# Kernel tuning notes

Hardware: AMD Instinct MI355X
Metric: run time of the kernel (lower is better)

## Reference

```python
import jax, jax.numpy as jnp
import numpy as np
from jax.ops import segment_sum

N_NODES = 50000
N_EDGES = 800000
D = 128
N_LAYERS = 3
N_GRAPHS = 256


def setup_inputs() -> dict:
    key = jax.random.key(0)
    k1, k2, k3, k4, k5, k6 = jax.random.split(key, 6)
    feats = jax.random.normal(k1, (N_NODES, D), dtype=jnp.float32)
    src = jax.random.randint(k2, (N_EDGES,), 0, N_NODES)
    dst = jax.random.randint(k3, (N_EDGES,), 0, N_NODES)
    graph_ids = jnp.sort(jax.random.randint(k4, (N_NODES,), 0, N_GRAPHS))
    W = jax.random.normal(k5, (N_LAYERS, D, D), dtype=jnp.float32) / np.float32(np.sqrt(D))
    b = jax.random.normal(k6, (N_LAYERS, D), dtype=jnp.float32) * 0.01
    return {"feats": feats, "W": W, "b": b, "src": src, "dst": dst, "graph_ids": graph_ids}


def reference(feats, W, b, src, dst, graph_ids):
    # DGL GraphConv with norm='both': h' = act(D_in^{-1/2} A D_out^{-1/2} h W + b)
    ones_e = jnp.ones((src.shape[0],), dtype=feats.dtype)
    deg_out = jnp.clip(segment_sum(ones_e, src, num_segments=N_NODES), 1.0)  # [N]
    deg_in = jnp.clip(segment_sum(ones_e, dst, num_segments=N_NODES), 1.0)   # [N]
    norm_out = jax.lax.rsqrt(deg_out)[:, None]  # [N,1]
    norm_in = jax.lax.rsqrt(deg_in)[:, None]    # [N,1]

    h = feats
    for l in range(N_LAYERS):
        hn = h * norm_out                                  # source-side norm
        agg = segment_sum(hn[src], dst, num_segments=N_NODES)  # SpMM gather/scatter
        agg = agg * norm_in                                # dest-side norm
        h = jax.nn.relu(agg @ W[l] + b[l])                 # [N,D]

    # AvgPooling readout: per-graph mean over nodes
    ones_n = jnp.ones((N_NODES,), dtype=h.dtype)
    counts = jnp.clip(segment_sum(ones_n, graph_ids, num_segments=N_GRAPHS), 1.0)
    pooled = segment_sum(h, graph_ids, num_segments=N_GRAPHS) / counts[:, None]
    return pooled  # [N_GRAPHS, D]
```

## Files before the change

### kernel.cpp

```cpp
#include <hip/hip_runtime.h>
#include <hip/hip_fp16.h>

#define DD 128
#define GG 256
#define RANGES 4
#define RSMAX 12544
#define NCHUNK 64

typedef _Float16 half8 __attribute__((ext_vector_type(8)));
typedef float floatx4 __attribute__((ext_vector_type(4)));

__device__ inline uint2 pack_half4(float4 v) {
    __half2 a = __floats2half2_rn(v.x, v.y);
    __half2 b = __floats2half2_rn(v.z, v.w);
    uint2 u;
    u.x = *reinterpret_cast<unsigned int*>(&a);
    u.y = *reinterpret_cast<unsigned int*>(&b);
    return u;
}

__global__ __launch_bounds__(256) void k_key(const int* __restrict__ src, const int* __restrict__ dst,
                                             unsigned int* __restrict__ key, int E) {
    int i = (blockIdx.x * 256 + threadIdx.x) * 4;
    if (i + 3 < E) {
        int4 s4 = *(const int4*)&src[i];
        int4 d4 = *(const int4*)&dst[i];
        uint4 k4;
        k4.x = (unsigned int)s4.x | ((unsigned int)d4.x << 16);
        k4.y = (unsigned int)s4.y | ((unsigned int)d4.y << 16);
        k4.z = (unsigned int)s4.z | ((unsigned int)d4.z << 16);
        k4.w = (unsigned int)s4.w | ((unsigned int)d4.w << 16);
        *(uint4*)&key[i] = k4;
    } else {
        for (int j = 0; j < 4 && i + j < E; ++j)
            key[i + j] = (unsigned int)src[i + j] | ((unsigned int)dst[i + j] << 16);
    }
}

__global__ __launch_bounds__(256) void k_hist2(const unsigned int* __restrict__ key,
                                               unsigned int* __restrict__ pk,
                                               int E, int N, int C, int RS, int L) {
    __shared__ unsigned int h[RSMAX];
    int r = blockIdx.x / C;
    int c = blockIdx.x % C;
    int r0 = r * RS;
    int r1 = min(r0 + RS, N);
    int nb = r1 - r0;
    for (int i = threadIdx.x; i < nb; i += 256) h[i] = 0;
    __syncthreads();
    int e0 = c * L, e1 = min(e0 + L, E);
    for (int e = e0 + threadIdx.x * 4; e < e1; e += 1024) {
        if (e + 3 < e1) {
            uint4 k4 = *(const uint4*)&key[e];
            #pragma unroll
            for (int j = 0; j < 4; ++j) {
                unsigned int kk = (j == 0) ? k4.x : (j == 1) ? k4.y : (j == 2) ? k4.z : k4.w;
                int s = (int)(kk & 0xFFFFu);
                int d = (int)(kk >> 16);
                if (s >= r0 && s < r1) atomicAdd(&h[s - r0], 1u);
                if (d >= r0 && d < r1) atomicAdd(&h[d - r0], 65536u);
            }
        } else {
            for (int j = 0; j < 4 && e + j < e1; ++j) {
                unsigned int kk = key[e + j];
                int s = (int)(kk & 0xFFFFu);
                int d = (int)(kk >> 16);
                if (s >= r0 && s < r1) atomicAdd(&h[s - r0], 1u);
                if (d >= r0 && d < r1) atomicAdd(&h[d - r0], 65536u);
            }
        }
    }
    __syncthreads();
    for (int i = threadIdx.x; i < nb; i += 256)
        pk[(size_t)c * N + r0 + i] = h[i];
}

__global__ __launch_bounds__(256) void k_reduce(const unsigned int* __restrict__ pk,
                                                float* __restrict__ norm_out, float* __restrict__ norm_in,
                                                int* __restrict__ deg_in, int* __restrict__ bsum,
                                                int N, int C) {
    __shared__ int ws[4];
    int n = blockIdx.x * 256 + threadIdx.x;
    int so = 0, si = 0;
    if (n < N) {
        for (int c = 0; c < C; ++c) {
            unsigned int v = pk[(size_t)c * N + n];
            so += (int)(v & 0xFFFFu);
            si += (int)(v >> 16);
        }
        norm_out[n] = rsqrtf(fmaxf((float)so, 1.0f));
        norm_in[n] = rsqrtf(fmaxf((float)si, 1.0f));
        deg_in[n] = si;
    }
    int s = si;
    #pragma unroll
    for (int off = 32; off; off >>= 1) s += __shfl_xor(s, off);
    int lane = threadIdx.x & 63, w = threadIdx.x >> 6;
    if (lane == 0) ws[w] = s;
    __syncthreads();
    if (threadIdx.x == 0) bsum[blockIdx.x] = ws[0] + ws[1] + ws[2] + ws[3];
}

__global__ __launch_bounds__(256) void k_misc(int* bsum, int nblk, int* row_ptr, int N,
                                              const int* __restrict__ gid, int* g_start, int G,
                                              const float* __restrict__ W, __half* __restrict__ Wt,
                                              const float* __restrict__ feats,
                                              const float* __restrict__ norm_out,
                                              uint2* __restrict__ Xh) {
    int blk = blockIdx.x;
    int tid = threadIdx.x;
    if (blk == 0) {
        if (tid < 64) {
            int lane = tid;
            int carry = 0;
            for (int base = 0; base < nblk; base += 64) {
                int i = base + lane;
                int v = (i < nblk) ? bsum[i] : 0;
                int s = v;
                #pragma unroll
                for (int off = 1; off < 64; off <<= 1) {
                    int u = __shfl_up(s, off);
                    if (lane >= off) s += u;
                }
                if (i < nblk) bsum[i] = carry + s - v;
                carry += __shfl(s, 63);
            }
            if (lane == 0) row_ptr[N] = carry;
        }
    } else if (blk <= 2) {
        int g = (blk - 1) * 256 + tid;
        if (g <= G) {
            int lo = 0, hi = N;
            while (lo < hi) {
                int mid = (lo + hi) >> 1;
                if (gid[mid] < g) lo = mid + 1; else hi = mid;
            }
            g_start[g] = lo;
        }
    } else if (blk <= 194) {
        int i = (blk - 3) * 256 + tid;
        if (i < 3 * 16384) {
            int l = i >> 14;
            int rem = i & 16383;
            int n = rem >> 7;
            int k = rem & 127;
            Wt[(size_t)l * 16384 + n * 128 + k] = __float2half(W[(size_t)l * 16384 + k * 128 + n]);
        }
    } else {
        int i = (blk - 195) * 256 + tid;
        if (i < N * 32) {
            int n = i >> 5;
            float4 v = ((const float4*)feats)[i];
            float s = norm_out[n];
            v.x *= s; v.y *= s; v.z *= s; v.w *= s;
            Xh[i] = pack_half4(v);
        }
    }
}

__global__ __launch_bounds__(256) void k_scan_cb(const int* __restrict__ deg, const int* __restrict__ bsum,
                                                 const unsigned int* __restrict__ pk,
                                                 int* __restrict__ row_ptr, int* __restrict__ fbase,
                                                 int N, int C) {
    __shared__ int ws[4];
    int t = threadIdx.x;
    int n = blockIdx.x * 256 + t;
    int v = (n < N) ? deg[n] : 0;
    int lane = t & 63, w = t >> 6;
    int incl = v;
    #pragma unroll
    for (int off = 1; off < 64; off <<= 1) {
        int u = __shfl_up(incl, off);
        if (lane >= off) incl += u;
    }
    if (lane == 63) ws[w] = incl;
    __syncthreads();
    int woff = 0;
    for (int j = 0; j < w; ++j) woff += ws[j];
    if (n < N) {
        int run = bsum[blockIdx.x] + woff + incl - v;
        row_ptr[n] = run;
        for (int c = 0; c < C; ++c) {
            int h = (int)(pk[(size_t)c * N + n] >> 16);
            fbase[(size_t)c * N + n] = run;
            run += h;
        }
    }
}

__global__ __launch_bounds__(256) void k_fill2(const unsigned int* __restrict__ key,
                                               const int* __restrict__ base, int* __restrict__ col_src,
                                               int E, int N, int C, int RS, int L) {
    __shared__ int cnt[RSMAX];
    int r = blockIdx.x / C;
    int c = blockIdx.x % C;
    int r0 = r * RS;
    int r1 = min(r0 + RS, N);
    int nb = r1 - r0;
    const int* bc = base + (size_t)c * N;
    for (int i = threadIdx.x; i < nb; i += 256) cnt[i] = bc[r0 + i];
    __syncthreads();
    int e0 = c * L, e1 = min(e0 + L, E);
    for (int e = e0 + threadIdx.x * 4; e < e1; e += 1024) {
        if (e + 3 < e1) {
            uint4 k4 = *(const uint4*)&key[e];
            #pragma unroll
            for (int j = 0; j < 4; ++j) {
                unsigned int kk = (j == 0) ? k4.x : (j == 1) ? k4.y : (j == 2) ? k4.z : k4.w;
                int s = (int)(kk & 0xFFFFu);
                int d = (int)(kk >> 16);
                if (d >= r0 && d < r1) { int o = atomicAdd(&cnt[d - r0], 1); col_src[o] = s; }
            }
        } else {
            for (int j = 0; j < 4 && e + j < e1; ++j) {
                unsigned int kk = key[e + j];
                int s = (int)(kk & 0xFFFFu);
                int d = (int)(kk >> 16);
                if (d >= r0 && d < r1) { int o = atomicAdd(&cnt[d - r0], 1); col_src[o] = s; }
            }
        }
    }
}

__device__ inline void acc_row(float* acc, uint4 u) {
    const __half2* h = (const __half2*)&u;
    #pragma unroll
    for (int i = 0; i < 4; ++i) {
        float2 f = __half22float2(h[i]);
        acc[2 * i] += f.x;
        acc[2 * i + 1] += f.y;
    }
}

__global__ __launch_bounds__(256, 8) void k_agg(const uint4* __restrict__ Xin, const float* __restrict__ norm_in,
                                                const int* __restrict__ row_ptr, const int* __restrict__ col_src,
                                                uint4* __restrict__ Yh, int N) {
    int t = threadIdx.x;
    int l16 = t & 15;
    int n = blockIdx.x * 16 + (t >> 4);
    if (n >= N) return;
    int beg = row_ptr[n], end = row_ptr[n + 1];
    float acc[8] = {};
    int k = beg;
    bool have = (k + 3 < end);
    int4 s = make_int4(0, 0, 0, 0);
    if (have) s = *(const int4*)&col_src[k];
    while (have) {
        int kn = k + 4;
        bool haven = (kn + 3 < end);
        int4 sn = s;
        if (haven) sn = *(const int4*)&col_src[kn];
        uint4 u0 = Xin[(size_t)s.x * 16 + l16];
        uint4 u1 = Xin[(size_t)s.y * 16 + l16];
        uint4 u2 = Xin[(size_t)s.z * 16 + l16];
        uint4 u3 = Xin[(size_t)s.w * 16 + l16];
        acc_row(acc, u0);
        acc_row(acc, u1);
        acc_row(acc, u2);
        acc_row(acc, u3);
        s = sn; k = kn; have = haven;
    }
    for (; k < end; ++k) {
        uint4 u = Xin[(size_t)col_src[k] * 16 + l16];
        acc_row(acc, u);
    }
    float ni = norm_in[n];
    #pragma unroll
    for (int i = 0; i < 8; ++i) acc[i] *= ni;
    __half2 hp[4];
    #pragma unroll
    for (int i = 0; i < 4; ++i) hp[i] = __floats2half2_rn(acc[2 * i], acc[2 * i + 1]);
    Yh[(size_t)n * 16 + l16] = *(uint4*)hp;
}

__global__ __launch_bounds__(256) void k_mm_mfma(const __half* __restrict__ Yh, const __half* __restrict__ Wt,
                                                 const float* __restrict__ bl, const float* __restrict__ scale,
                                                 float* __restrict__ outf, __half* __restrict__ outh, int N) {
    __shared__ _Float16 Ah[128 * 136];
    __shared__ _Float16 Bt[128 * 136];
    int tid = threadIdx.x;
    int n0 = blockIdx.x * 128;

    for (int q = tid; q < 2048; q += 256) {
        int rr = q >> 4, cc = q & 15;
        int node = n0 + rr;
        float4 v = make_float4(0.f, 0.f, 0.f, 0.f);
        if (node < N) v = *(const float4*)&Yh[(size_t)node * 128 + cc * 8];
        *(float4*)&Ah[rr * 136 + cc * 8] = v;
        *(float4*)&Bt[rr * 136 + cc * 8] = *(const float4*)&Wt[(size_t)rr * 128 + cc * 8];
    }
    __syncthreads();

    int wave = tid >> 6;
    int lane = tid & 63;
    int quad = lane >> 4;
    int mrow = lane & 15;
    int m0 = wave * 32;

    half8 af[2][4];
    #pragma unroll
    for (int sub = 0; sub < 2; ++sub)
        #pragma unroll
        for (int kc = 0; kc < 4; ++kc)
            af[sub][kc] = *(const half8*)&Ah[(m0 + sub * 16 + mrow) * 136 + kc * 32 + quad * 8];

    floatx4 acc[2][8];
    #pragma unroll
    for (int sub = 0; sub < 2; ++sub)
        #pragma unroll
        for (int ct = 0; ct < 8; ++ct) acc[sub][ct] = (floatx4){0.f, 0.f, 0.f, 0.f};

    #pragma unroll
    for (int ct = 0; ct < 8; ++ct) {
        #pragma unroll
        for (int kc = 0; kc < 4; ++kc) {
            half8 bf = *(const half8*)&Bt[(ct * 16 + mrow) * 136 + kc * 32 + quad * 8];
            acc[0][ct] = __builtin_amdgcn_mfma_f32_16x16x32_f16(af[0][kc], bf, acc[0][ct], 0, 0, 0);
            acc[1][ct] = __builtin_amdgcn_mfma_f32_16x16x32_f16(af[1][kc], bf, acc[1][ct], 0, 0, 0);
        }
    }

    #pragma unroll
    for (int sub = 0; sub < 2; ++sub) {
        float sc[4];
        #pragma unroll
        for (int r = 0; r < 4; ++r) {
            int node = n0 + m0 + sub * 16 + quad * 4 + r;
            sc[r] = (scale && node < N) ? scale[node] : 1.0f;
        }
        #pragma unroll
        for (int ct = 0; ct < 8; ++ct) {
            int col = ct * 16 + mrow;
            float bias = bl[col];
            #pragma unroll
            for (int r = 0; r < 4; ++r) {
                int node = n0 + m0 + sub * 16 + quad * 4 + r;
                if (node < N) {
                    float val = fmaxf(acc[sub][ct][r] + bias, 0.f);
                    if (outh) outh[(size_t)node * 128 + col] = __float2half(val * sc[r]);
                    else outf[(size_t)node * 128 + col] = val;
                }
            }
        }
    }
}

__global__ __launch_bounds__(256) void k_pool(const __half2* __restrict__ Fh, const int* __restrict__ g_start,
                                              float* __restrict__ out) {
    __shared__ float2 red[4][64];
    int g = blockIdx.x;
    int t = threadIdx.x;
    int cp = t & 63;
    int nl = t >> 6;
    int beg = g_start[g], end = g_start[g + 1];
    float2 acc = make_float2(0.f, 0.f);
    for (int n = beg + nl; n < end; n += 4) {
        float2 f = __half22float2(Fh[(size_t)n * 64 + cp]);
        acc.x += f.x;
        acc.y += f.y;
    }
    red[nl][cp] = acc;
    __syncthreads();
    if (nl == 0) {
        float2 a0 = red[0][cp], a1 = red[1][cp], a2 = red[2][cp], a3 = red[3][cp];
        float cnt = fmaxf((float)(end - beg), 1.0f);
        float2 o;
        o.x = (a0.x + a1.x + a2.x + a3.x) / cnt;
        o.y = (a0.y + a1.y + a2.y + a3.y) / cnt;
        *(float2*)&out[(size_t)g * DD + cp * 2] = o;
    }
}

extern "C" void kernel_launch(void* const* d_in, const int* in_sizes, int n_in,
                              void* d_out, int out_size, void* d_ws, size_t ws_size,
                              hipStream_t stream) {
    const float* feats = (const float*)d_in[0];
    const float* W = (const float*)d_in[1];
    const float* b = (const float*)d_in[2];
    const int* src = (const int*)d_in[3];
    const int* dst = (const int*)d_in[4];
    const int* gid = (const int*)d_in[5];
    float* out = (float*)d_out;
    const int N = in_sizes[0] / DD;
    const int E = in_sizes[3];

    const int C = NCHUNK;
    const int RS = (N + RANGES - 1) / RANGES;
    const int L = (((E + C - 1) / C) + 3) & ~3;

    char* ws = (char*)d_ws;
    size_t off = 0;
    auto take = [&](size_t bytes) {
        char* p = ws + off;
        off = (off + bytes + 255) & ~(size_t)255;
        return p;
    };
    float* norm_out = (float*)take((size_t)N * 4);
    float* norm_in  = (float*)take((size_t)N * 4);
    int*   deg_in   = (int*)take((size_t)N * 4);
    int*   row_ptr  = (int*)take((size_t)(N + 1) * 4);
    int*   col_src  = (int*)take((size_t)E * 4);
    int*   g_start  = (int*)take((size_t)(GG + 1) * 4);
    int*   bsum     = (int*)take((size_t)1024 * 4);
    unsigned int* key = (unsigned int*)take((size_t)E * 4);
    __half* Wth     = (__half*)take((size_t)3 * 16384 * 2);
    uint4* Xh       = (uint4*)take((size_t)N * DD * 2);
    uint4* Yh       = (uint4*)take((size_t)N * DD * 2);
    size_t chunk_arr = ((size_t)C * N * 4 + 255) & ~(size_t)255;
    size_t uni_bytes = 2 * chunk_arr;
    size_t fh_bytes = (size_t)N * DD * 2;
    char* uni = take(uni_bytes > fh_bytes ? uni_bytes : fh_bytes);
    unsigned int* pk = (unsigned int*)uni;
    int* fbase = (int*)(uni + chunk_arr);
    __half* Fh = (__half*)uni;

    const int nblk = (N + 255) / 256;
    const int mgrid_misc = 195 + (N * 32 + 255) / 256;

    k_key<<<(E + 1023) / 1024, 256, 0, stream>>>(src, dst, key, E);
    k_hist2<<<RANGES * C, 256, 0, stream>>>(key, pk, E, N, C, RS, L);
    k_reduce<<<nblk, 256, 0, stream>>>(pk, norm_out, norm_in, deg_in, bsum, N, C);
    k_misc<<<mgrid_misc, 256, 0, stream>>>(bsum, nblk, row_ptr, N, gid, g_start, GG,
                                           W, Wth, feats, norm_out, (uint2*)Xh);
    k_scan_cb<<<nblk, 256, 0, stream>>>(deg_in, bsum, pk, row_ptr, fbase, N, C);
    k_fill2<<<RANGES * C, 256, 0, stream>>>(key, fbase, col_src, E, N, C, RS, L);

    const int agrid = (N + 15) / 16;
    const int mgrid = (N + 127) / 128;
    for (int l = 0; l < 3; ++l) {
        k_agg<<<agrid, 256, 0, stream>>>(Xh, norm_in, row_ptr, col_src, Yh, N);
        const __half* Wtl = Wth + (size_t)l * 16384;
        const float* bl = b + (size_t)l * DD;
        if (l < 2)
            k_mm_mfma<<<mgrid, 256, 0, stream>>>((const __half*)Yh, Wtl, bl, norm_out,
                                                 nullptr, (__half*)Xh, N);
        else
            k_mm_mfma<<<mgrid, 256, 0, stream>>>((const __half*)Yh, Wtl, bl, nullptr,
                                                 nullptr, Fh, N);
    }
    k_pool<<<GG, 256, 0, stream>>>((const __half2*)Fh, g_start, out);
}
```

Measured before the change: 301.4 us.

## Fuse aggregation, dense matmul, and average pooling into one per-layer kernel

Each 16-node block now gathers its neighbour rows, stages the aggregated tile in shared memory, and multiplies it by W with MFMA directly, reading W fragments from global memory. This drops the Yh round trip and the separate matmul launch. On the last layer the bias and ReLU output is reduced per graph and atomically added into the output, which is zeroed in the scan kernel, replacing the standalone pooling kernel and the Fh buffer. The cost is that every block reloads the full W from global or L2 instead of sharing it across 128-row tiles, and the pooling now depends on float atomics.

```diff
diff --git a/kernel.cpp b/kernel.cpp
--- a/kernel.cpp
+++ b/kernel.cpp
@@ -161,9 +161,14 @@
 __global__ __launch_bounds__(256) void k_scan_cb(const int* __restrict__ deg, const int* __restrict__ bsum,
                                                  const unsigned int* __restrict__ pk,
                                                  int* __restrict__ row_ptr, int* __restrict__ fbase,
+                                                 float* __restrict__ pool0,
                                                  int N, int C) {
     __shared__ int ws[4];
     int t = threadIdx.x;
+    if (blockIdx.x < 32) {
+        float4 z = make_float4(0.f, 0.f, 0.f, 0.f);
+        ((float4*)pool0)[blockIdx.x * 256 + t] = z;
+    }
     int n = blockIdx.x * 256 + t;
     int v = (n < N) ? deg[n] : 0;
     int lane = t & 63, w = t >> 6;
@@ -232,142 +237,152 @@
     }
 }
 
-__global__ __launch_bounds__(256, 8) void k_agg(const uint4* __restrict__ Xin, const float* __restrict__ norm_in,
-                                                const int* __restrict__ row_ptr, const int* __restrict__ col_src,
-                                                uint4* __restrict__ Yh, int N) {
+__global__ __launch_bounds__(256, 8) void k_agg_mm(
+    const uint4* __restrict__ Xin, const float* __restrict__ norm_in,
+    const int* __restrict__ row_ptr, const int* __restrict__ col_src,
+    const __half* __restrict__ Wt, const float* __restrict__ bl,
+    const float* __restrict__ scale, __half* __restrict__ Xout,
+    float* __restrict__ pool_out, const int* __restrict__ gid,
+    const int* __restrict__ g_start, int N) {
+    __shared__ _Float16 Ah[16 * 136];
     int t = threadIdx.x;
+    int n0 = blockIdx.x * 16;
     int l16 = t & 15;
-    int n = blockIdx.x * 16 + (t >> 4);
-    if (n >= N) return;
-    int beg = row_ptr[n], end = row_ptr[n + 1];
+    int grp = t >> 4;
+    int n = n0 + grp;
+
     float acc[8] = {};
-    int k = beg;
-    bool have = (k + 3 < end);
-    int4 s = make_int4(0, 0, 0, 0);
-    if (have) s = *(const int4*)&col_src[k];
-    while (have) {
-        int kn = k + 4;
-        bool haven = (kn + 3 < end);
-        int4 sn = s;
-        if (haven) sn = *(const int4*)&col_src[kn];
-        uint4 u0 = Xin[(size_t)s.x * 16 + l16];
-        uint4 u1 = Xin[(size_t)s.y * 16 + l16];
-        uint4 u2 = Xin[(size_t)s.z * 16 + l16];
-        uint4 u3 = Xin[(size_t)s.w * 16 + l16];
-        acc_row(acc, u0);
-        acc_row(acc, u1);
-        acc_row(acc, u2);
-        acc_row(acc, u3);
-        s = sn; k = kn; have = haven;
-    }
-    for (; k < end; ++k) {
-        uint4 u = Xin[(size_t)col_src[k] * 16 + l16];
-        acc_row(acc, u);
-    }
-    float ni = norm_in[n];
-    #pragma unroll
-    for (int i = 0; i < 8; ++i) acc[i] *= ni;
+    if (n < N) {
+        int beg = row_ptr[n], end = row_ptr[n + 1];
+        int k = beg;
+        bool have = (k + 3 < end);
+        int4 s = make_int4(0, 0, 0, 0);
+        if (have) s = *(const int4*)&col_src[k];
+        while (have) {
+            int kn = k + 4;
+            bool haven = (kn + 3 < end);
+            int4 sn = s;
+            if (haven) sn = *(const int4*)&col_src[kn];
+            uint4 u0 = Xin[(size_t)s.x * 16 + l16];
+            uint4 u1 = Xin[(size_t)s.y * 16 + l16];
+            uint4 u2 = Xin[(size_t)s.z * 16 + l16];
+            uint4 u3 = Xin[(size_t)s.w * 16 + l16];
+            acc_row(acc, u0);
+            acc_row(acc, u1);
+            acc_row(acc, u2);
+            acc_row(acc, u3);
+            s = sn; k = kn; have = haven;
+        }
+        for (; k < end; ++k) {
+            uint4 u = Xin[(size_t)col_src[k] * 16 + l16];
+            acc_row(acc, u);
+        }
+        float ni = norm_in[n];
+        #pragma unroll
+        for (int i = 0; i < 8; ++i) acc[i] *= ni;
+    }
     __half2 hp[4];
     #pragma unroll
     for (int i = 0; i < 4; ++i) hp[i] = __floats2half2_rn(acc[2 * i], acc[2 * i + 1]);
-    Yh[(size_t)n * 16 + l16] = *(uint4*)hp;
-}
-
-__global__ __launch_bounds__(256) void k_mm_mfma(const __half* __restrict__ Yh, const __half* __restrict__ Wt,
-                                                 const float* __restrict__ bl, const float* __restrict__ scale,
-                                                 float* __restrict__ outf, __half* __restrict__ outh, int N) {
-    __shared__ _Float16 Ah[128 * 136];
-    __shared__ _Float16 Bt[128 * 136];
-    int tid = threadIdx.x;
-    int n0 = blockIdx.x * 128;
-
-    for (int q = tid; q < 2048; q += 256) {
-        int rr = q >> 4, cc = q & 15;
-        int node = n0 + rr;
-        float4 v = make_float4(0.f, 0.f, 0.f, 0.f);
-        if (node < N) v = *(const float4*)&Yh[(size_t)node * 128 + cc * 8];
-        *(float4*)&Ah[rr * 136 + cc * 8] = v;
-        *(float4*)&Bt[rr * 136 + cc * 8] = *(const float4*)&Wt[(size_t)rr * 128 + cc * 8];
-    }
-    __syncthreads();
-
-    int wave = tid >> 6;
-    int lane = tid & 63;
+    *(uint4*)&Ah[grp * 136 + l16 * 8] = *(const uint4*)hp;
+    __syncthreads();
+
+    int wave = t >> 6;
+    int lane = t & 63;
     int quad = lane >> 4;
     int mrow = lane & 15;
-    int m0 = wave * 32;
-
-    half8 af[2][4];
-    #pragma unroll
-    for (int sub = 0; sub < 2; ++sub)
-        #pragma unroll
-        for (int kc = 0; kc < 4; ++kc)
-            af[sub][kc] = *(const half8*)&Ah[(m0 + sub * 16 + mrow) * 136 + kc * 32 + quad * 8];
-
-    floatx4 acc[2][8];
-    #pragma unroll
-    for (int sub = 0; sub < 2; ++sub)
-        #pragma unroll
-        for (int ct = 0; ct < 8; ++ct) acc[sub][ct] = (floatx4){0.f, 0.f, 0.f, 0.f};
-
-    #pragma unroll
-    for (int ct = 0; ct < 8; ++ct) {
+
+    half8 af[4];
+    #pragma unroll
+    for (int kc = 0; kc < 4; ++kc)
+        af[kc] = *(const half8*)&Ah[mrow * 136 + kc * 32 + quad * 8];
+
+    floatx4 Cc[2];
+    Cc[0] = (floatx4){0.f, 0.f, 0.f, 0.f};
+    Cc[1] = (floatx4){0.f, 0.f, 0.f, 0.f};
+    #pragma unroll
+    for (int ct = 0; ct < 2; ++ct) {
+        int col = wave * 32 + ct * 16 + mrow;
         #pragma unroll
         for (int kc = 0; kc < 4; ++kc) {
-            half8 bf = *(const half8*)&Bt[(ct * 16 + mrow) * 136 + kc * 32 + quad * 8];
-            acc[0][ct] = __builtin_amdgcn_mfma_f32_16x16x32_f16(af[0][kc], bf, acc[0][ct], 0, 0, 0);
-            acc[1][ct] = __builtin_amdgcn_mfma_f32_16x16x32_f16(af[1][kc], bf, acc[1][ct], 0, 0, 0);
-        }
-    }
-
-    #pragma unroll
-    for (int sub = 0; sub < 2; ++sub) {
+            half8 bf = *(const half8*)&Wt[(size_t)col * 128 + kc * 32 + quad * 8];
+            Cc[ct] = __builtin_amdgcn_mfma_f32_16x16x32_f16(af[kc], bf, Cc[ct], 0, 0, 0);
+        }
+    }
+
+    if (Xout) {
         float sc[4];
         #pragma unroll
         for (int r = 0; r < 4; ++r) {
-            int node = n0 + m0 + sub * 16 + quad * 4 + r;
-            sc[r] = (scale && node < N) ? scale[node] : 1.0f;
+            int node = n0 + quad * 4 + r;
+            sc[r] = (node < N) ? scale[node] : 1.0f;
         }
         #pragma unroll
-        for (int ct = 0; ct < 8; ++ct) {
-            int col = ct * 16 + mrow;
+        for (int ct = 0; ct < 2; ++ct) {
+            int col = wave * 32 + ct * 16 + mrow;
             float bias = bl[col];
             #pragma unroll
             for (int r = 0; r < 4; ++r) {
-                int node = n0 + m0 + sub * 16 + quad * 4 + r;
-                if (node < N) {
-                    float val = fmaxf(acc[sub][ct][r] + bias, 0.f);
-                    if (outh) outh[(size_t)node * 128 + col] = __float2half(val * sc[r]);
-                    else outf[(size_t)node * 128 + col] = val;
+                int node = n0 + quad * 4 + r;
+                if (node < N)
+                    Xout[(size_t)node * 128 + col] =
+                        __float2half(fmaxf(Cc[ct][r] + bias, 0.f) * sc[r]);
+            }
+        }
+    } else {
+        int nlast = min(n0 + 15, N - 1);
+        int ga = (n0 < N) ? gid[n0] : -1;
+        int gb = (n0 < N) ? gid[nlast] : -2;
+        if (ga == gb && ga >= 0) {
+            float inv = 1.f / fmaxf((float)(g_start[ga + 1] - g_start[ga]), 1.f);
+            #pragma unroll
+            for (int ct = 0; ct < 2; ++ct) {
+                int col = wave * 32 + ct * 16 + mrow;
+                float bias = bl[col];
+                float s = 0.f;
+                #pragma unroll
+                for (int r = 0; r < 4; ++r) {
+                    int node = n0 + quad * 4 + r;
+                    if (node < N) s += fmaxf(Cc[ct][r] + bias, 0.f);
                 }
-            }
-        }
-    }
-}
-
-__global__ __launch_bounds__(256) void k_pool(const __half2* __restrict__ Fh, const int* __restrict__ g_start,
-                                              float* __restrict__ out) {
-    __shared__ float2 red[4][64];
-    int g = blockIdx.x;
-    int t = threadIdx.x;
-    int cp = t & 63;
-    int nl = t >> 6;
-    int beg = g_start[g], end = g_start[g + 1];
-    float2 acc = make_float2(0.f, 0.f);
-    for (int n = beg + nl; n < end; n += 4) {
-        float2 f = __half22float2(Fh[(size_t)n * 64 + cp]);
-        acc.x += f.x;
-        acc.y += f.y;
-    }
-    red[nl][cp] = acc;
-    __syncthreads();
-    if (nl == 0) {
-        float2 a0 = red[0][cp], a1 = red[1][cp], a2 = red[2][cp], a3 = red[3][cp];
-        float cnt = fmaxf((float)(end - beg), 1.0f);
-        float2 o;
-        o.x = (a0.x + a1.x + a2.x + a3.x) / cnt;
-        o.y = (a0.y + a1.y + a2.y + a3.y) / cnt;
-        *(float2*)&out[(size_t)g * DD + cp * 2] = o;
+                s += __shfl_xor(s, 16);
+                s += __shfl_xor(s, 32);
+                if (quad == 0) atomicAdd(&pool_out[(size_t)ga * DD + col], s * inv);
+            }
+        } else {
+            int garr[4];
+            #pragma unroll
+            for (int r = 0; r < 4; ++r) {
+                int node = n0 + quad * 4 + r;
+                garr[r] = (node < N) ? gid[node] : -1;
+            }
+            #pragma unroll
+            for (int ct = 0; ct < 2; ++ct) {
+                int col = wave * 32 + ct * 16 + mrow;
+                float bias = bl[col];
+                float s = 0.f;
+                int gcur = -1;
+                #pragma unroll
+                for (int r = 0; r < 4; ++r) {
+                    if (garr[r] >= 0) {
+                        float val = fmaxf(Cc[ct][r] + bias, 0.f);
+                        if (garr[r] != gcur) {
+                            if (gcur >= 0) {
+                                float cnt = fmaxf((float)(g_start[gcur + 1] - g_start[gcur]), 1.f);
+                                atomicAdd(&pool_out[(size_t)gcur * DD + col], s / cnt);
+                            }
+                            gcur = garr[r];
+                            s = 0.f;
+                        }
+                        s += val;
+                    }
+                }
+                if (gcur >= 0) {
+                    float cnt = fmaxf((float)(g_start[gcur + 1] - g_start[gcur]), 1.f);
+                    atomicAdd(&pool_out[(size_t)gcur * DD + col], s / cnt);
+                }
+            }
+        }
     }
 }
 
@@ -407,12 +422,9 @@
     uint4* Xh       = (uint4*)take((size_t)N * DD * 2);
     uint4* Yh       = (uint4*)take((size_t)N * DD * 2);
     size_t chunk_arr = ((size_t)C * N * 4 + 255) & ~(size_t)255;
-    size_t uni_bytes = 2 * chunk_arr;
-    size_t fh_bytes = (size_t)N * DD * 2;
-    char* uni = take(uni_bytes > fh_bytes ? uni_bytes : fh_bytes);
+    char* uni = take(2 * chunk_arr);
     unsigned int* pk = (unsigned int*)uni;
     int* fbase = (int*)(uni + chunk_arr);
-    __half* Fh = (__half*)uni;
 
     const int nblk = (N + 255) / 256;
     const int mgrid_misc = 195 + (N * 32 + 255) / 256;
@@ -422,21 +434,21 @@
     k_reduce<<<nblk, 256, 0, stream>>>(pk, norm_out, norm_in, deg_in, bsum, N, C);
     k_misc<<<mgrid_misc, 256, 0, stream>>>(bsum, nblk, row_ptr, N, gid, g_start, GG,
                                            W, Wth, feats, norm_out, (uint2*)Xh);
-    k_scan_cb<<<nblk, 256, 0, stream>>>(deg_in, bsum, pk, row_ptr, fbase, N, C);
+    k_scan_cb<<<nblk, 256, 0, stream>>>(deg_in, bsum, pk, row_ptr, fbase, out, N, C);
     k_fill2<<<RANGES * C, 256, 0, stream>>>(key, fbase, col_src, E, N, C, RS, L);
 
     const int agrid = (N + 15) / 16;
-    const int mgrid = (N + 127) / 128;
     for (int l = 0; l < 3; ++l) {
-        k_agg<<<agrid, 256, 0, stream>>>(Xh, norm_in, row_ptr, col_src, Yh, N);
         const __half* Wtl = Wth + (size_t)l * 16384;
-        const float* bl = b + (size_t)l * DD;
-        if (l < 2)
-            k_mm_mfma<<<mgrid, 256, 0, stream>>>((const __half*)Yh, Wtl, bl, norm_out,
-                                                 nullptr, (__half*)Xh, N);
-        else
-            k_mm_mfma<<<mgrid, 256, 0, stream>>>((const __half*)Yh, Wtl, bl, nullptr,
-                                                 nullptr, Fh, N);
-    }
-    k_pool<<<GG, 256, 0, stream>>>((const __half2*)Fh, g_start, out);
-}
+        const float* blp = b + (size_t)l * DD;
+        const uint4* Xi = (l == 1) ? Yh : Xh;
+        if (l < 2) {
+            __half* Xo = (__half*)((l == 0) ? Yh : Xh);
+            k_agg_mm<<<agrid, 256, 0, stream>>>(Xi, norm_in, row_ptr, col_src, Wtl, blp,
+                                                norm_out, Xo, nullptr, nullptr, nullptr, N);
+        } else {
+            k_agg_mm<<<agrid, 256, 0, stream>>>(Xi, norm_in, row_ptr, col_src, Wtl, blp,
+                                                nullptr, nullptr, out, gid, g_start, N);
+        }
+    }
+}
```

After: 264.2 us, median of 2. 1.14x faster.

## Split fp16 features into column quarters and pin quarters to XCDs for gather

Applied to the files above, without the earlier changes.

Node features are now stored as four column slices of 32 halves each, and the aggregation kernel is rewritten so each block handles one slice for 64 nodes. Block indices are arranged so that each slice maps to a fixed pair of XCDs. A given L2 then only ever sees one slice, roughly a quarter of the feature table, which should cut misses on the random source-row gathers. The edge-index loads and output stores become nontemporal, and the matmul kernel reads and writes the sliced layout in place. The cost is four times as many reads of the edge list and narrower per-node loads.

```diff
diff --git a/kernel.cpp b/kernel.cpp
--- a/kernel.cpp
+++ b/kernel.cpp
@@ -9,6 +9,8 @@
 
 typedef _Float16 half8 __attribute__((ext_vector_type(8)));
 typedef float floatx4 __attribute__((ext_vector_type(4)));
+typedef int intv4 __attribute__((ext_vector_type(4)));
+typedef unsigned int uintv4 __attribute__((ext_vector_type(4)));
 
 __device__ inline uint2 pack_half4(float4 v) {
     __half2 a = __floats2half2_rn(v.x, v.y);
@@ -106,7 +108,7 @@
                                               const float* __restrict__ W, __half* __restrict__ Wt,
                                               const float* __restrict__ feats,
                                               const float* __restrict__ norm_out,
-                                              uint2* __restrict__ Xh) {
+                                              __half* __restrict__ Xq) {
     int blk = blockIdx.x;
     int tid = threadIdx.x;
     if (blk == 0) {
@@ -150,10 +152,14 @@
         int i = (blk - 195) * 256 + tid;
         if (i < N * 32) {
             int n = i >> 5;
+            int c4 = i & 31;
             float4 v = ((const float4*)feats)[i];
             float s = norm_out[n];
             v.x *= s; v.y *= s; v.z *= s; v.w *= s;
-            Xh[i] = pack_half4(v);
+            int col0 = c4 * 4;
+            int qq = col0 >> 5;
+            size_t hidx = (size_t)qq * N * 32 + (size_t)n * 32 + (col0 & 31);
+            *(uint2*)&Xq[hidx] = pack_half4(v);
         }
     }
 }
@@ -222,38 +228,45 @@
     }
 }
 
-__device__ inline void acc_row(float* acc, uint4 u) {
-    const __half2* h = (const __half2*)&u;
+__device__ inline void acc_row(float* acc, uintv4 u) {
     #pragma unroll
     for (int i = 0; i < 4; ++i) {
-        float2 f = __half22float2(h[i]);
+        unsigned int w = u[i];
+        __half2 h = *reinterpret_cast<const __half2*>(&w);
+        float2 f = __half22float2(h);
         acc[2 * i] += f.x;
         acc[2 * i + 1] += f.y;
     }
 }
 
-__global__ __launch_bounds__(256, 8) void k_agg(const uint4* __restrict__ Xin, const float* __restrict__ norm_in,
-                                                const int* __restrict__ row_ptr, const int* __restrict__ col_src,
-                                                uint4* __restrict__ Yh, int N) {
-    int t = threadIdx.x;
-    int l16 = t & 15;
-    int n = blockIdx.x * 16 + (t >> 4);
+__global__ __launch_bounds__(256, 8) void k_agg_q(
+    const uintv4* __restrict__ Xq, const float* __restrict__ norm_in,
+    const int* __restrict__ row_ptr, const int* __restrict__ col_src,
+    uintv4* __restrict__ Yq, int N) {
+    int x = blockIdx.x & 7;
+    int t = blockIdx.x >> 3;
+    int q = x >> 1;
+    int tile = t * 2 + (x & 1);
+    int n = tile * 64 + (threadIdx.x >> 2);
+    int l4 = threadIdx.x & 3;
     if (n >= N) return;
+    const uintv4* Xs = Xq + (size_t)q * N * 4;
+
     int beg = row_ptr[n], end = row_ptr[n + 1];
     float acc[8] = {};
     int k = beg;
     bool have = (k + 3 < end);
-    int4 s = make_int4(0, 0, 0, 0);
-    if (have) s = *(const int4*)&col_src[k];
+    intv4 s = (intv4){0, 0, 0, 0};
+    if (have) s = __builtin_nontemporal_load((const intv4*)&col_src[k]);
     while (have) {
         int kn = k + 4;
         bool haven = (kn + 3 < end);
-        int4 sn = s;
-        if (haven) sn = *(const int4*)&col_src[kn];
-        uint4 u0 = Xin[(size_t)s.x * 16 + l16];
-        uint4 u1 = Xin[(size_t)s.y * 16 + l16];
-        uint4 u2 = Xin[(size_t)s.z * 16 + l16];
-        uint4 u3 = Xin[(size_t)s.w * 16 + l16];
+        intv4 sn = s;
+        if (haven) sn = __builtin_nontemporal_load((const intv4*)&col_src[kn]);
+        uintv4 u0 = Xs[(size_t)s.x * 4 + l4];
+        uintv4 u1 = Xs[(size_t)s.y * 4 + l4];
+        uintv4 u2 = Xs[(size_t)s.z * 4 + l4];
+        uintv4 u3 = Xs[(size_t)s.w * 4 + l4];
         acc_row(acc, u0);
         acc_row(acc, u1);
         acc_row(acc, u2);
@@ -261,7 +274,7 @@
         s = sn; k = kn; have = haven;
     }
     for (; k < end; ++k) {
-        uint4 u = Xin[(size_t)col_src[k] * 16 + l16];
+        uintv4 u = Xs[(size_t)col_src[k] * 4 + l4];
         acc_row(acc, u);
     }
     float ni = norm_in[n];
@@ -270,24 +283,29 @@
     __half2 hp[4];
     #pragma unroll
     for (int i = 0; i < 4; ++i) hp[i] = __floats2half2_rn(acc[2 * i], acc[2 * i + 1]);
-    Yh[(size_t)n * 16 + l16] = *(uint4*)hp;
-}
-
-__global__ __launch_bounds__(256) void k_mm_mfma(const __half* __restrict__ Yh, const __half* __restrict__ Wt,
-                                                 const float* __restrict__ bl, const float* __restrict__ scale,
-                                                 float* __restrict__ outf, __half* __restrict__ outh, int N) {
+    uintv4 pv;
+    #pragma unroll
+    for (int i = 0; i < 4; ++i) pv[i] = *reinterpret_cast<unsigned int*>(&hp[i]);
+    __builtin_nontemporal_store(pv, &Yq[(size_t)q * N * 4 + (size_t)n * 4 + l4]);
+}
+
+__global__ __launch_bounds__(256) void k_mm_q(const __half* __restrict__ Yin, const __half* __restrict__ Wt,
+                                              const float* __restrict__ bl, const float* __restrict__ scale,
+                                              __half* __restrict__ Yout, __half* __restrict__ Fh, int N) {
     __shared__ _Float16 Ah[128 * 136];
     __shared__ _Float16 Bt[128 * 136];
     int tid = threadIdx.x;
     int n0 = blockIdx.x * 128;
 
-    for (int q = tid; q < 2048; q += 256) {
-        int rr = q >> 4, cc = q & 15;
+    for (int idx = tid; idx < 2048; idx += 256) {
+        int rr = idx >> 4, cc = idx & 15;
         int node = n0 + rr;
+        int col0 = cc * 8;
         float4 v = make_float4(0.f, 0.f, 0.f, 0.f);
-        if (node < N) v = *(const float4*)&Yh[(size_t)node * 128 + cc * 8];
-        *(float4*)&Ah[rr * 136 + cc * 8] = v;
-        *(float4*)&Bt[rr * 136 + cc * 8] = *(const float4*)&Wt[(size_t)rr * 128 + cc * 8];
+        if (node < N)
+            v = *(const float4*)&Yin[(size_t)(col0 >> 5) * N * 32 + (size_t)node * 32 + (col0 & 31)];
+        *(float4*)&Ah[rr * 136 + col0] = v;
+        *(float4*)&Bt[rr * 136 + col0] = *(const float4*)&Wt[(size_t)rr * 128 + col0];
     }
     __syncthreads();
 
@@ -337,8 +355,12 @@
                 int node = n0 + m0 + sub * 16 + quad * 4 + r;
                 if (node < N) {
                     float val = fmaxf(acc[sub][ct][r] + bias, 0.f);
-                    if (outh) outh[(size_t)node * 128 + col] = __float2half(val * sc[r]);
-                    else outf[(size_t)node * 128 + col] = val;
+                    if (Fh) {
+                        Fh[(size_t)node * 128 + col] = __float2half(val);
+                    } else {
+                        Yout[(size_t)(col >> 5) * N * 32 + (size_t)node * 32 + (col & 31)] =
+                            __float2half(val * sc[r]);
+                    }
                 }
             }
         }
@@ -404,12 +426,10 @@
     int*   bsum     = (int*)take((size_t)1024 * 4);
     unsigned int* key = (unsigned int*)take((size_t)E * 4);
     __half* Wth     = (__half*)take((size_t)3 * 16384 * 2);
-    uint4* Xh       = (uint4*)take((size_t)N * DD * 2);
-    uint4* Yh       = (uint4*)take((size_t)N * DD * 2);
+    __half* Xq      = (__half*)take((size_t)N * DD * 2);
+    __half* Yq      = (__half*)take((size_t)N * DD * 2);
     size_t chunk_arr = ((size_t)C * N * 4 + 255) & ~(size_t)255;
-    size_t uni_bytes = 2 * chunk_arr;
-    size_t fh_bytes = (size_t)N * DD * 2;
-    char* uni = take(uni_bytes > fh_bytes ? uni_bytes : fh_bytes);
+    char* uni = take(2 * chunk_arr);
     unsigned int* pk = (unsigned int*)uni;
     int* fbase = (int*)(uni + chunk_arr);
     __half* Fh = (__half*)uni;
@@ -421,22 +441,23 @@
     k_hist2<<<RANGES * C, 256, 0, stream>>>(key, pk, E, N, C, RS, L);
     k_reduce<<<nblk, 256, 0, stream>>>(pk, norm_out, norm_in, deg_in, bsum, N, C);
     k_misc<<<mgrid_misc, 256, 0, stream>>>(bsum, nblk, row_ptr, N, gid, g_start, GG,
-                                           W, Wth, feats, norm_out, (uint2*)Xh);
+                                           W, Wth, feats, norm_out, Xq);
     k_scan_cb<<<nblk, 256, 0, stream>>>(deg_in, bsum, pk, row_ptr, fbase, N, C);
     k_fill2<<<RANGES * C, 256, 0, stream>>>(key, fbase, col_src, E, N, C, RS, L);
 
-    const int agrid = (N + 15) / 16;
-    const int mgrid = (N + 127) / 128;
-    for (int l = 0; l < 3; ++l) {
-        k_agg<<<agrid, 256, 0, stream>>>(Xh, norm_in, row_ptr, col_src, Yh, N);
-        const __half* Wtl = Wth + (size_t)l * 16384;
-        const float* bl = b + (size_t)l * DD;
-        if (l < 2)
-            k_mm_mfma<<<mgrid, 256, 0, stream>>>((const __half*)Yh, Wtl, bl, norm_out,
-                                                 nullptr, (__half*)Xh, N);
-        else
-            k_mm_mfma<<<mgrid, 256, 0, stream>>>((const __half*)Yh, Wtl, bl, nullptr,
-                                                 nullptr, Fh, N);
-    }
+    const int tiles = (N + 63) / 64;
+    const int tpairs = (tiles + 1) / 2;
+    const int qa_grid = tpairs * 8;
+    const int mm_grid = (N + 127) / 128;
+
+    k_agg_q<<<qa_grid, 256, 0, stream>>>((const uintv4*)Xq, norm_in, row_ptr, col_src,
+                                         (uintv4*)Yq, N);
+    k_mm_q<<<mm_grid, 256, 0, stream>>>(Yq, Wth, b, norm_out, Yq, nullptr, N);
+    k_agg_q<<<qa_grid, 256, 0, stream>>>((const uintv4*)Yq, norm_in, row_ptr, col_src,
+                                         (uintv4*)Xq, N);
+    k_mm_q<<<mm_grid, 256, 0, stream>>>(Xq, Wth + 16384, b + DD, norm_out, Xq, nullptr, N);
+    k_agg_q<<<qa_grid, 256, 0, stream>>>((const uintv4*)Xq, norm_in, row_ptr, col_src,
+                                         (uintv4*)Yq, N);
+    k_mm_q<<<mm_grid, 256, 0, stream>>>(Yq, Wth + 2 * 16384, b + 2 * DD, nullptr, nullptr, Fh, N);
     k_pool<<<GG, 256, 0, stream>>>((const __half2*)Fh, g_start, out);
 }
```

After: 323.1 us. +7.2%, slower.
